# Optimization experiments

Measured on AMD Instinct MI355X. Metric: run time of the kernel, lower is better.

## Reference

```python
import jax, jax.numpy as jnp
import numpy as np

N = 50000
H = 256
EPS = 1e-5

def setup_inputs() -> dict:
    key = jax.random.key(0)
    ks = jax.random.split(key, 8)
    d = 128
    inp = {
        'x': jax.random.normal(ks[0], (N, d), jnp.float32),
        'edge_index': jax.random.randint(ks[1], (2, 800000), 0, N, jnp.int64),
        'W1': jax.random.normal(ks[2], (d, H), jnp.float32) * (2.0 / d) ** 0.5,
        'b1': jnp.zeros((H,), jnp.float32),
        'g1': jnp.ones((H,), jnp.float32),
        'be1': jnp.zeros((H,), jnp.float32),
        'W2': jax.random.normal(ks[3], (H, H), jnp.float32) * (2.0 / H) ** 0.5,
        'b2': jnp.zeros((H,), jnp.float32),
        'g2': jnp.ones((H,), jnp.float32),
        'be2': jnp.zeros((H,), jnp.float32),
        'W3': jax.random.normal(ks[4], (H, H), jnp.float32) * (2.0 / H) ** 0.5,
        'b3': jnp.zeros((H,), jnp.float32),
        'g3': jnp.ones((H,), jnp.float32),
        'be3': jnp.zeros((H,), jnp.float32),
        'Wf1': jax.random.normal(ks[5], (H, H // 2), jnp.float32) * (2.0 / H) ** 0.5,
        'bf1': jnp.zeros((H // 2,), jnp.float32),
        'Wf2': jax.random.normal(ks[6], (H // 2, 1), jnp.float32) * (2.0 / (H // 2)) ** 0.5,
        'bf2': jnp.zeros((1,), jnp.float32),
    }
    return inp

def _gcn_norm(edge_index):
    # add self-loops, symmetric normalization (PyG GCNConv defaults)
    loop = jnp.arange(N, dtype=edge_index.dtype)
    row = jnp.concatenate([edge_index[0], loop])  # source
    col = jnp.concatenate([edge_index[1], loop])  # target
    deg = jax.ops.segment_sum(jnp.ones_like(col, jnp.float32), col, num_segments=N)
    dis = jnp.where(deg > 0, jax.lax.rsqrt(deg), 0.0)
    norm = dis[row] * dis[col]  # [E+N]
    return row, col, norm

def _conv(x, W, b, row, col, norm):
    xw = x @ W                       # [N,H]
    msg = xw[row] * norm[:, None]    # gather + scale, [E+N,H]
    out = jax.ops.segment_sum(msg, col, num_segments=N)
    return out + b

def _ln(x, g, b):
    mu = jnp.mean(x, axis=-1, keepdims=True)
    var = jnp.var(x, axis=-1, keepdims=True)
    return (x - mu) * jax.lax.rsqrt(var + EPS) * g + b

def reference(x, edge_index, W1, b1, g1, be1, W2, b2, g2, be2, W3, b3, g3, be3, Wf1, bf1, Wf2, bf2):
    row, col, norm = _gcn_norm(edge_index)
    x1 = jax.nn.relu(_ln(_conv(x, W1, b1, row, col, norm), g1, be1))
    x2 = jax.nn.relu(_ln(_conv(x1, W2, b2, row, col, norm), g2, be2)) + 0.7 * x1
    x3 = jax.nn.relu(_ln(_conv(x2, W3, b3, row, col, norm), g3, be3)) * 0.7 + x2
    h = jax.nn.relu(x3 @ Wf1 + bf1)
    return h @ Wf2 + bf2  # [N,1]
```

## Files before the change

### kernel.cpp

```cpp
#include <hip/hip_runtime.h>
#include <cstdint>
#include <cstddef>

#define HDIM 256
#define DIN 128
#define EPSV 1e-5f
#define SCHUNK 1024

typedef __attribute__((ext_vector_type(8))) short short8;
typedef __attribute__((ext_vector_type(4))) float f32x4;

__device__ __forceinline__ float bf2f(unsigned int u16) {
  union { unsigned int i; float f; } v; v.i = u16 << 16; return v.f;
}
__device__ __forceinline__ unsigned short f2bf(float f) {
  union { float f; unsigned int i; } v; v.f = f;
  unsigned int u = v.i;
  return (unsigned short)((u + 0x7fffu + ((u >> 16) & 1u)) >> 16);
}
__device__ __forceinline__ float4 ldbf4(const unsigned short* p) {
  uint2 v = *(const uint2*)p;
  return make_float4(bf2f(v.x & 0xffffu), bf2f(v.x >> 16),
                     bf2f(v.y & 0xffffu), bf2f(v.y >> 16));
}
__device__ __forceinline__ void stbf4(unsigned short* p, float a, float b, float c, float d) {
  uint2 o;
  o.x = (unsigned int)f2bf(a) | ((unsigned int)f2bf(b) << 16);
  o.y = (unsigned int)f2bf(c) | ((unsigned int)f2bf(d) << 16);
  *(uint2*)p = o;
}

__global__ __launch_bounds__(256) void zero_i_k(int* deg, int* cur, int n) {
  int i = blockIdx.x * 256 + threadIdx.x;
  if (i < n) { deg[i] = 0; cur[i] = 0; }
}

__global__ __launch_bounds__(256) void hist_k(const int* __restrict__ col, int* deg, int e) {
  int i = blockIdx.x * 256 + threadIdx.x;
  if (i < e) atomicAdd(&deg[col[i]], 1);
}

__global__ __launch_bounds__(256) void scanA_k(const int* __restrict__ deg,
                                               int* __restrict__ row_ptr,
                                               int* __restrict__ blockSums,
                                               float* __restrict__ dis, int n) {
  __shared__ int waveSums[4];
  const int tid = threadIdx.x, lane = tid & 63, w = tid >> 6;
  const int base = blockIdx.x * SCHUNK + tid * 4;
  int v0 = 0, v1 = 0, v2 = 0, v3 = 0;
  if (base + 0 < n) v0 = deg[base + 0];
  if (base + 1 < n) v1 = deg[base + 1];
  if (base + 2 < n) v2 = deg[base + 2];
  if (base + 3 < n) v3 = deg[base + 3];
  if (base + 0 < n) dis[base + 0] = rsqrtf((float)(v0 + 1));
  if (base + 1 < n) dis[base + 1] = rsqrtf((float)(v1 + 1));
  if (base + 2 < n) dis[base + 2] = rsqrtf((float)(v2 + 1));
  if (base + 3 < n) dis[base + 3] = rsqrtf((float)(v3 + 1));
  int tsum = v0 + v1 + v2 + v3;
  int inc = tsum;
#pragma unroll
  for (int off = 1; off < 64; off <<= 1) {
    int t = __shfl_up(inc, off);
    if (lane >= off) inc += t;
  }
  if (lane == 63) waveSums[w] = inc;
  __syncthreads();
  int woff = 0;
#pragma unroll
  for (int k = 0; k < 4; ++k) woff += (k < w) ? waveSums[k] : 0;
  int excl = woff + inc - tsum;
  if (base + 0 < n) row_ptr[base + 0] = excl;
  if (base + 1 < n) row_ptr[base + 1] = excl + v0;
  if (base + 2 < n) row_ptr[base + 2] = excl + v0 + v1;
  if (base + 3 < n) row_ptr[base + 3] = excl + v0 + v1 + v2;
  if (tid == 255) blockSums[blockIdx.x] = woff + inc;
}

__global__ __launch_bounds__(256) void scanB_k(int* blockSums, int nb) {
  __shared__ int waveSums[4];
  const int tid = threadIdx.x, lane = tid & 63, w = tid >> 6;
  int v = (tid < nb) ? blockSums[tid] : 0;
  int inc = v;
#pragma unroll
  for (int off = 1; off < 64; off <<= 1) {
    int t = __shfl_up(inc, off);
    if (lane >= off) inc += t;
  }
  if (lane == 63) waveSums[w] = inc;
  __syncthreads();
  int woff = 0;
#pragma unroll
  for (int k = 0; k < 4; ++k) woff += (k < w) ? waveSums[k] : 0;
  if (tid < nb) blockSums[tid] = woff + inc - v;
}

__global__ __launch_bounds__(256) void scanC_k(int* __restrict__ row_ptr,
                                               const int* __restrict__ blockSums,
                                               int n, int e) {
  const int base = blockIdx.x * SCHUNK + threadIdx.x * 4;
  const int add = blockSums[blockIdx.x];
#pragma unroll
  for (int k = 0; k < 4; ++k)
    if (base + k < n) row_ptr[base + k] += add;
  if (blockIdx.x == 0 && threadIdx.x == 0) row_ptr[n] = e;
}

__global__ __launch_bounds__(256) void fill_k(const int* __restrict__ row,
                                              const int* __restrict__ col,
                                              const int* __restrict__ row_ptr,
                                              int* cur, int* srcs, int e) {
  int i = blockIdx.x * 256 + threadIdx.x;
  if (i < e) {
    int c = col[i];
    int p = row_ptr[c] + atomicAdd(&cur[c], 1);
    srcs[p] = row[i];
  }
}

__global__ __launch_bounds__(256) void pack_k(const float* __restrict__ W,
                                              unsigned short* __restrict__ out,
                                              int K, int C) {
  int idx = blockIdx.x * 256 + threadIdx.x;
  if (idx >= K * C) return;
  int j = idx & 7, lane = (idx >> 3) & 63, rest = idx >> 9;
  int NSUB = C >> 4;
  int ns = rest % NSUB, kb = rest / NSUB;
  int k = kb * 32 + (lane >> 4) * 8 + j;
  int c = ns * 16 + (lane & 15);
  out[idx] = f2bf(W[(size_t)k * C + c]);
}

__global__ __launch_bounds__(256) void cvt_k(const float* __restrict__ in,
                                             unsigned short* __restrict__ out, int tot) {
  int i = blockIdx.x * 256 + threadIdx.x;
  if (i < tot) out[i] = f2bf(in[i]);
}

template<int MODE, int K, int CN>
__global__ __launch_bounds__(256) void gemm_k(
    const unsigned short* __restrict__ A, const unsigned short* __restrict__ Wp,
    unsigned short* __restrict__ out, const float* __restrict__ sb, int n) {
  constexpr int NSUB = CN / 16;
  constexpr int KC = K / 32;
  const int t = threadIdx.x;
  const int w = t >> 6, lane = t & 63;
  const int rg = w & 1, cg = w >> 1;
  const int g = lane >> 4, i = lane & 15;
  const int m0 = blockIdx.x * 64 + rg * 32;
  const int nsBase = blockIdx.y * 8 + cg * 4;

  const int r0 = m0 + i, r1 = m0 + 16 + i;
  const int l0 = r0 < n ? r0 : n - 1;
  const int l1 = r1 < n ? r1 : n - 1;
  const unsigned short* a0 = A + (size_t)l0 * K + g * 8;
  const unsigned short* a1 = A + (size_t)l1 * K + g * 8;
  const short8* wp = (const short8*)Wp + (size_t)nsBase * 64 + lane;

  f32x4 acc[2][4];
#pragma unroll
  for (int rr = 0; rr < 2; ++rr)
#pragma unroll
    for (int j = 0; j < 4; ++j) acc[rr][j] = (f32x4){0.f, 0.f, 0.f, 0.f};

  short8 af0 = *(const short8*)a0;
  short8 af1 = *(const short8*)a1;
  short8 wf[4];
#pragma unroll
  for (int j = 0; j < 4; ++j) wf[j] = wp[j * 64];

#pragma unroll
  for (int kc = 0; kc < KC; ++kc) {
    short8 naf0, naf1, nwf[4];
    if (kc + 1 < KC) {
      naf0 = *(const short8*)(a0 + (kc + 1) * 32);
      naf1 = *(const short8*)(a1 + (kc + 1) * 32);
#pragma unroll
      for (int j = 0; j < 4; ++j) nwf[j] = wp[(size_t)(kc + 1) * NSUB * 64 + j * 64];
    }
#pragma unroll
    for (int j = 0; j < 4; ++j) {
      acc[0][j] = __builtin_amdgcn_mfma_f32_16x16x32_bf16(wf[j], af0, acc[0][j], 0, 0, 0);
      acc[1][j] = __builtin_amdgcn_mfma_f32_16x16x32_bf16(wf[j], af1, acc[1][j], 0, 0, 0);
    }
    if (kc + 1 < KC) {
      af0 = naf0; af1 = naf1;
#pragma unroll
      for (int j = 0; j < 4; ++j) wf[j] = nwf[j];
    }
  }

#pragma unroll
  for (int rr = 0; rr < 2; ++rr) {
    int r = m0 + rr * 16 + i;
    if (r < n) {
      unsigned short* op = out + (size_t)r * CN + nsBase * 16 + g * 4;
      if (MODE == 0) {
        float s = sb[r];
#pragma unroll
        for (int j = 0; j < 4; ++j)
          stbf4(op + j * 16, acc[rr][j][0] * s, acc[rr][j][1] * s,
                acc[rr][j][2] * s, acc[rr][j][3] * s);
      } else {
#pragma unroll
        for (int j = 0; j < 4; ++j) {
          float4 b4 = *(const float4*)(sb + nsBase * 16 + j * 16 + g * 4);
          stbf4(op + j * 16,
                fmaxf(acc[rr][j][0] + b4.x, 0.f), fmaxf(acc[rr][j][1] + b4.y, 0.f),
                fmaxf(acc[rr][j][2] + b4.z, 0.f), fmaxf(acc[rr][j][3] + b4.w, 0.f));
        }
      }
    }
  }
}

template<int MODE>
__global__ __launch_bounds__(256) void gather_ln_k(
    const unsigned short* __restrict__ xws, const int* __restrict__ row_ptr,
    const int* __restrict__ srcs, const float* __restrict__ dis,
    const float* __restrict__ bias, const float* __restrict__ g,
    const float* __restrict__ be, const unsigned short* __restrict__ xprev,
    unsigned short* __restrict__ out, int n) {
  int i = blockIdx.x * 4 + (threadIdx.x >> 6);
  int lane = threadIdx.x & 63;
  if (i >= n) return;
  int beg = row_ptr[i], end = row_ptr[i + 1];
  const int co = lane * 4;
  float4 acc = ldbf4(xws + (size_t)i * HDIM + co);
  int j = beg;
  for (; j + 8 <= end; j += 8) {
    int r0 = srcs[j], r1 = srcs[j + 1], r2 = srcs[j + 2], r3 = srcs[j + 3];
    int r4 = srcs[j + 4], r5 = srcs[j + 5], r6 = srcs[j + 6], r7 = srcs[j + 7];
    float4 v0 = ldbf4(xws + (size_t)r0 * HDIM + co);
    float4 v1 = ldbf4(xws + (size_t)r1 * HDIM + co);
    float4 v2 = ldbf4(xws + (size_t)r2 * HDIM + co);
    float4 v3 = ldbf4(xws + (size_t)r3 * HDIM + co);
    float4 v4 = ldbf4(xws + (size_t)r4 * HDIM + co);
    float4 v5 = ldbf4(xws + (size_t)r5 * HDIM + co);
    float4 v6 = ldbf4(xws + (size_t)r6 * HDIM + co);
    float4 v7 = ldbf4(xws + (size_t)r7 * HDIM + co);
    acc.x += ((v0.x + v1.x) + (v2.x + v3.x)) + ((v4.x + v5.x) + (v6.x + v7.x));
    acc.y += ((v0.y + v1.y) + (v2.y + v3.y)) + ((v4.y + v5.y) + (v6.y + v7.y));
    acc.z += ((v0.z + v1.z) + (v2.z + v3.z)) + ((v4.z + v5.z) + (v6.z + v7.z));
    acc.w += ((v0.w + v1.w) + (v2.w + v3.w)) + ((v4.w + v5.w) + (v6.w + v7.w));
  }
  for (; j + 4 <= end; j += 4) {
    int r0 = srcs[j], r1 = srcs[j + 1], r2 = srcs[j + 2], r3 = srcs[j + 3];
    float4 v0 = ldbf4(xws + (size_t)r0 * HDIM + co);
    float4 v1 = ldbf4(xws + (size_t)r1 * HDIM + co);
    float4 v2 = ldbf4(xws + (size_t)r2 * HDIM + co);
    float4 v3 = ldbf4(xws + (size_t)r3 * HDIM + co);
    acc.x += (v0.x + v1.x) + (v2.x + v3.x);
    acc.y += (v0.y + v1.y) + (v2.y + v3.y);
    acc.z += (v0.z + v1.z) + (v2.z + v3.z);
    acc.w += (v0.w + v1.w) + (v2.w + v3.w);
  }
  for (; j < end; ++j) {
    float4 v = ldbf4(xws + (size_t)srcs[j] * HDIM + co);
    acc.x += v.x; acc.y += v.y; acc.z += v.z; acc.w += v.w;
  }
  float di = dis[i];
  float4 b4 = *(const float4*)(bias + co);
  float4 v;
  v.x = acc.x * di + b4.x;
  v.y = acc.y * di + b4.y;
  v.z = acc.z * di + b4.z;
  v.w = acc.w * di + b4.w;
  float s = v.x + v.y + v.z + v.w;
  float s2 = v.x * v.x + v.y * v.y + v.z * v.z + v.w * v.w;
#pragma unroll
  for (int off = 1; off < 64; off <<= 1) {
    s += __shfl_xor(s, off);
    s2 += __shfl_xor(s2, off);
  }
  float mu = s * (1.f / HDIM);
  float inv = rsqrtf(s2 * (1.f / HDIM) - mu * mu + EPSV);
  float4 g4 = *(const float4*)(g + co);
  float4 e4 = *(const float4*)(be + co);
  float4 o;
  o.x = fmaxf((v.x - mu) * inv * g4.x + e4.x, 0.f);
  o.y = fmaxf((v.y - mu) * inv * g4.y + e4.y, 0.f);
  o.z = fmaxf((v.z - mu) * inv * g4.z + e4.z, 0.f);
  o.w = fmaxf((v.w - mu) * inv * g4.w + e4.w, 0.f);
  if (MODE == 1) {
    float4 p = ldbf4(xprev + (size_t)i * HDIM + co);
    o.x += 0.7f * p.x; o.y += 0.7f * p.y; o.z += 0.7f * p.z; o.w += 0.7f * p.w;
  } else if (MODE == 2) {
    float4 p = ldbf4(xprev + (size_t)i * HDIM + co);
    o.x = o.x * 0.7f + p.x; o.y = o.y * 0.7f + p.y;
    o.z = o.z * 0.7f + p.z; o.w = o.w * 0.7f + p.w;
  }
  stbf4(out + (size_t)i * HDIM + co, o.x, o.y, o.z, o.w);
}

__global__ __launch_bounds__(256) void dot_k(
    const unsigned short* __restrict__ h, const float* __restrict__ w,
    const float* __restrict__ bf2, float* __restrict__ out, int n) {
  int i = blockIdx.x * 4 + (threadIdx.x >> 6);
  int lane = threadIdx.x & 63;
  if (i >= n) return;
  unsigned int hv = *(const unsigned int*)(h + (size_t)i * 128 + lane * 2);
  float2 wv = *(const float2*)(w + lane * 2);
  float p = bf2f(hv & 0xffffu) * wv.x + bf2f(hv >> 16) * wv.y;
#pragma unroll
  for (int off = 1; off < 64; off <<= 1) p += __shfl_xor(p, off);
  if (lane == 0) out[i] = p + bf2[0];
}

extern "C" void kernel_launch(void* const* d_in, const int* in_sizes, int n_in,
                              void* d_out, int out_size, void* d_ws, size_t ws_size,
                              hipStream_t stream) {
  const float* x   = (const float*)d_in[0];
  const int*   ei  = (const int*)d_in[1];
  const float* W1  = (const float*)d_in[2];
  const float* b1  = (const float*)d_in[3];
  const float* g1  = (const float*)d_in[4];
  const float* be1 = (const float*)d_in[5];
  const float* W2  = (const float*)d_in[6];
  const float* b2  = (const float*)d_in[7];
  const float* g2  = (const float*)d_in[8];
  const float* be2 = (const float*)d_in[9];
  const float* W3  = (const float*)d_in[10];
  const float* b3  = (const float*)d_in[11];
  const float* g3  = (const float*)d_in[12];
  const float* be3 = (const float*)d_in[13];
  const float* Wf1 = (const float*)d_in[14];
  const float* bf1 = (const float*)d_in[15];
  const float* Wf2 = (const float*)d_in[16];
  const float* bf2 = (const float*)d_in[17];
  float* out = (float*)d_out;

  const int n = in_sizes[0] / DIN;
  const int e = in_sizes[1] / 2;
  const int* row = ei;
  const int* col = ei + e;

  char* ws = (char*)d_ws;
  size_t off = 0;
  auto alloc = [&](size_t bytes) -> void* {
    void* p = ws + off;
    off = (off + bytes + 255) & ~(size_t)255;
    return p;
  };
  float*          dis     = (float*)alloc((size_t)n * 4);
  int*            deg_i   = (int*)alloc((size_t)n * 4);
  int*            cur     = (int*)alloc((size_t)n * 4);
  int*            row_ptr = (int*)alloc((size_t)(n + 1) * 4);
  int*            bsums   = (int*)alloc((size_t)256 * 4);
  int*            srcs    = (int*)alloc((size_t)e * 4);
  unsigned short* W1p     = (unsigned short*)alloc((size_t)DIN * HDIM * 2);
  unsigned short* W2p     = (unsigned short*)alloc((size_t)HDIM * HDIM * 2);
  unsigned short* W3p     = (unsigned short*)alloc((size_t)HDIM * HDIM * 2);
  unsigned short* Wf1p    = (unsigned short*)alloc((size_t)HDIM * 128 * 2);
  unsigned short* xbf     = (unsigned short*)alloc((size_t)n * DIN * 2);
  unsigned short* xws     = (unsigned short*)alloc((size_t)n * HDIM * 2);
  unsigned short* x1      = (unsigned short*)alloc((size_t)n * HDIM * 2);
  unsigned short* x2      = (unsigned short*)alloc((size_t)n * HDIM * 2);
  unsigned short* x3      = x1;
  unsigned short* h       = xbf;

  const int nb  = (n + 255) / 256;
  const int eb  = (e + 255) / 256;
  const int lnb = (n + 3) / 4;
  const int sb_ = (n + SCHUNK - 1) / SCHUNK;
  dim3 gg((n + 63) / 64, 2);
  dim3 gh((n + 63) / 64, 1);

  zero_i_k<<<nb, 256, 0, stream>>>(deg_i, cur, n);
  hist_k<<<eb, 256, 0, stream>>>(col, deg_i, e);
  scanA_k<<<sb_, 256, 0, stream>>>(deg_i, row_ptr, bsums, dis, n);
  scanB_k<<<1, 256, 0, stream>>>(bsums, sb_);
  scanC_k<<<sb_, 256, 0, stream>>>(row_ptr, bsums, n, e);
  fill_k<<<eb, 256, 0, stream>>>(row, col, row_ptr, cur, srcs, e);

  pack_k<<<(DIN * HDIM + 255) / 256, 256, 0, stream>>>(W1, W1p, DIN, HDIM);
  pack_k<<<(HDIM * HDIM + 255) / 256, 256, 0, stream>>>(W2, W2p, HDIM, HDIM);
  pack_k<<<(HDIM * HDIM + 255) / 256, 256, 0, stream>>>(W3, W3p, HDIM, HDIM);
  pack_k<<<(HDIM * 128 + 255) / 256, 256, 0, stream>>>(Wf1, Wf1p, HDIM, 128);
  cvt_k<<<(n * DIN + 255) / 256, 256, 0, stream>>>(x, xbf, n * DIN);

  gemm_k<0, DIN, HDIM><<<gg, 256, 0, stream>>>(xbf, W1p, xws, dis, n);
  gather_ln_k<0><<<lnb, 256, 0, stream>>>(xws, row_ptr, srcs, dis, b1, g1, be1, nullptr, x1, n);

  gemm_k<0, HDIM, HDIM><<<gg, 256, 0, stream>>>(x1, W2p, xws, dis, n);
  gather_ln_k<1><<<lnb, 256, 0, stream>>>(xws, row_ptr, srcs, dis, b2, g2, be2, x1, x2, n);

  gemm_k<0, HDIM, HDIM><<<gg, 256, 0, stream>>>(x2, W3p, xws, dis, n);
  gather_ln_k<2><<<lnb, 256, 0, stream>>>(xws, row_ptr, srcs, dis, b3, g3, be3, x2, x3, n);

  gemm_k<1, HDIM, 128><<<gh, 256, 0, stream>>>(x3, Wf1p, h, bf1, n);
  dot_k<<<lnb, 256, 0, stream>>>(h, Wf2, bf2, out, n);
}
```

Baseline: 486.2 us.

## Aggregate before GEMM and fuse LayerNorm and final MLP into GEMM epilogues

```diff
diff --git a/kernel.cpp b/kernel.cpp
--- a/kernel.cpp
+++ b/kernel.cpp
@@ -117,11 +117,9 @@
   }
 }
 
-__global__ __launch_bounds__(256) void pack_k(const float* __restrict__ W,
-                                              unsigned short* __restrict__ out,
-                                              int K, int C) {
-  int idx = blockIdx.x * 256 + threadIdx.x;
-  if (idx >= K * C) return;
+__device__ __forceinline__ void packW(const float* __restrict__ W,
+                                      unsigned short* __restrict__ out,
+                                      int idx, int C) {
   int j = idx & 7, lane = (idx >> 3) & 63, rest = idx >> 9;
   int NSUB = C >> 4;
   int ns = rest % NSUB, kb = rest / NSUB;
@@ -130,180 +128,285 @@
   out[idx] = f2bf(W[(size_t)k * C + c]);
 }
 
-__global__ __launch_bounds__(256) void cvt_k(const float* __restrict__ in,
-                                             unsigned short* __restrict__ out, int tot) {
-  int i = blockIdx.x * 256 + threadIdx.x;
-  if (i < tot) out[i] = f2bf(in[i]);
-}
-
-template<int MODE, int K, int CN>
-__global__ __launch_bounds__(256) void gemm_k(
-    const unsigned short* __restrict__ A, const unsigned short* __restrict__ Wp,
-    unsigned short* __restrict__ out, const float* __restrict__ sb, int n) {
-  constexpr int NSUB = CN / 16;
-  constexpr int KC = K / 32;
-  const int t = threadIdx.x;
-  const int w = t >> 6, lane = t & 63;
-  const int rg = w & 1, cg = w >> 1;
-  const int g = lane >> 4, i = lane & 15;
-  const int m0 = blockIdx.x * 64 + rg * 32;
-  const int nsBase = blockIdx.y * 8 + cg * 4;
-
-  const int r0 = m0 + i, r1 = m0 + 16 + i;
-  const int l0 = r0 < n ? r0 : n - 1;
-  const int l1 = r1 < n ? r1 : n - 1;
-  const unsigned short* a0 = A + (size_t)l0 * K + g * 8;
-  const unsigned short* a1 = A + (size_t)l1 * K + g * 8;
-  const short8* wp = (const short8*)Wp + (size_t)nsBase * 64 + lane;
-
-  f32x4 acc[2][4];
-#pragma unroll
-  for (int rr = 0; rr < 2; ++rr)
-#pragma unroll
-    for (int j = 0; j < 4; ++j) acc[rr][j] = (f32x4){0.f, 0.f, 0.f, 0.f};
-
-  short8 af0 = *(const short8*)a0;
-  short8 af1 = *(const short8*)a1;
-  short8 wf[4];
-#pragma unroll
-  for (int j = 0; j < 4; ++j) wf[j] = wp[j * 64];
-
-#pragma unroll
-  for (int kc = 0; kc < KC; ++kc) {
-    short8 naf0, naf1, nwf[4];
-    if (kc + 1 < KC) {
-      naf0 = *(const short8*)(a0 + (kc + 1) * 32);
-      naf1 = *(const short8*)(a1 + (kc + 1) * 32);
-#pragma unroll
-      for (int j = 0; j < 4; ++j) nwf[j] = wp[(size_t)(kc + 1) * NSUB * 64 + j * 64];
-    }
-#pragma unroll
-    for (int j = 0; j < 4; ++j) {
-      acc[0][j] = __builtin_amdgcn_mfma_f32_16x16x32_bf16(wf[j], af0, acc[0][j], 0, 0, 0);
-      acc[1][j] = __builtin_amdgcn_mfma_f32_16x16x32_bf16(wf[j], af1, acc[1][j], 0, 0, 0);
-    }
-    if (kc + 1 < KC) {
-      af0 = naf0; af1 = naf1;
-#pragma unroll
-      for (int j = 0; j < 4; ++j) wf[j] = nwf[j];
-    }
-  }
-
-#pragma unroll
-  for (int rr = 0; rr < 2; ++rr) {
-    int r = m0 + rr * 16 + i;
-    if (r < n) {
-      unsigned short* op = out + (size_t)r * CN + nsBase * 16 + g * 4;
-      if (MODE == 0) {
-        float s = sb[r];
-#pragma unroll
-        for (int j = 0; j < 4; ++j)
-          stbf4(op + j * 16, acc[rr][j][0] * s, acc[rr][j][1] * s,
-                acc[rr][j][2] * s, acc[rr][j][3] * s);
-      } else {
-#pragma unroll
-        for (int j = 0; j < 4; ++j) {
-          float4 b4 = *(const float4*)(sb + nsBase * 16 + j * 16 + g * 4);
-          stbf4(op + j * 16,
-                fmaxf(acc[rr][j][0] + b4.x, 0.f), fmaxf(acc[rr][j][1] + b4.y, 0.f),
-                fmaxf(acc[rr][j][2] + b4.z, 0.f), fmaxf(acc[rr][j][3] + b4.w, 0.f));
-        }
-      }
-    }
-  }
-}
-
-template<int MODE>
-__global__ __launch_bounds__(256) void gather_ln_k(
-    const unsigned short* __restrict__ xws, const int* __restrict__ row_ptr,
+__global__ __launch_bounds__(256) void prep_k(
+    const float* __restrict__ W1, const float* __restrict__ W2,
+    const float* __restrict__ W3, const float* __restrict__ Wf1,
+    const float* __restrict__ x,
+    unsigned short* __restrict__ W1p, unsigned short* __restrict__ W2p,
+    unsigned short* __restrict__ W3p, unsigned short* __restrict__ Wf1p,
+    unsigned short* __restrict__ xbf, int nx) {
+  int idx = blockIdx.x * 256 + threadIdx.x;
+  const int s0 = DIN * HDIM, s1 = s0 + HDIM * HDIM, s2 = s1 + HDIM * HDIM,
+            s3 = s2 + HDIM * 128;
+  if (idx < s0) packW(W1, W1p, idx, HDIM);
+  else if (idx < s1) packW(W2, W2p, idx - s0, HDIM);
+  else if (idx < s2) packW(W3, W3p, idx - s1, HDIM);
+  else if (idx < s3) packW(Wf1, Wf1p, idx - s2, 128);
+  else if (idx - s3 < nx) xbf[idx - s3] = f2bf(x[idx - s3]);
+}
+
+__global__ __launch_bounds__(256) void gather256_k(
+    const unsigned short* __restrict__ x, const int* __restrict__ row_ptr,
     const int* __restrict__ srcs, const float* __restrict__ dis,
-    const float* __restrict__ bias, const float* __restrict__ g,
-    const float* __restrict__ be, const unsigned short* __restrict__ xprev,
     unsigned short* __restrict__ out, int n) {
   int i = blockIdx.x * 4 + (threadIdx.x >> 6);
   int lane = threadIdx.x & 63;
   if (i >= n) return;
   int beg = row_ptr[i], end = row_ptr[i + 1];
   const int co = lane * 4;
-  float4 acc = ldbf4(xws + (size_t)i * HDIM + co);
+  float di = dis[i];
+  float4 sv = ldbf4(x + (size_t)i * 256 + co);
+  float4 acc = make_float4(di * sv.x, di * sv.y, di * sv.z, di * sv.w);
   int j = beg;
   for (; j + 8 <= end; j += 8) {
     int r0 = srcs[j], r1 = srcs[j + 1], r2 = srcs[j + 2], r3 = srcs[j + 3];
     int r4 = srcs[j + 4], r5 = srcs[j + 5], r6 = srcs[j + 6], r7 = srcs[j + 7];
-    float4 v0 = ldbf4(xws + (size_t)r0 * HDIM + co);
-    float4 v1 = ldbf4(xws + (size_t)r1 * HDIM + co);
-    float4 v2 = ldbf4(xws + (size_t)r2 * HDIM + co);
-    float4 v3 = ldbf4(xws + (size_t)r3 * HDIM + co);
-    float4 v4 = ldbf4(xws + (size_t)r4 * HDIM + co);
-    float4 v5 = ldbf4(xws + (size_t)r5 * HDIM + co);
-    float4 v6 = ldbf4(xws + (size_t)r6 * HDIM + co);
-    float4 v7 = ldbf4(xws + (size_t)r7 * HDIM + co);
-    acc.x += ((v0.x + v1.x) + (v2.x + v3.x)) + ((v4.x + v5.x) + (v6.x + v7.x));
-    acc.y += ((v0.y + v1.y) + (v2.y + v3.y)) + ((v4.y + v5.y) + (v6.y + v7.y));
-    acc.z += ((v0.z + v1.z) + (v2.z + v3.z)) + ((v4.z + v5.z) + (v6.z + v7.z));
-    acc.w += ((v0.w + v1.w) + (v2.w + v3.w)) + ((v4.w + v5.w) + (v6.w + v7.w));
-  }
-  for (; j + 4 <= end; j += 4) {
-    int r0 = srcs[j], r1 = srcs[j + 1], r2 = srcs[j + 2], r3 = srcs[j + 3];
-    float4 v0 = ldbf4(xws + (size_t)r0 * HDIM + co);
-    float4 v1 = ldbf4(xws + (size_t)r1 * HDIM + co);
-    float4 v2 = ldbf4(xws + (size_t)r2 * HDIM + co);
-    float4 v3 = ldbf4(xws + (size_t)r3 * HDIM + co);
-    acc.x += (v0.x + v1.x) + (v2.x + v3.x);
-    acc.y += (v0.y + v1.y) + (v2.y + v3.y);
-    acc.z += (v0.z + v1.z) + (v2.z + v3.z);
-    acc.w += (v0.w + v1.w) + (v2.w + v3.w);
+    float d0 = dis[r0], d1 = dis[r1], d2 = dis[r2], d3 = dis[r3];
+    float d4 = dis[r4], d5 = dis[r5], d6 = dis[r6], d7 = dis[r7];
+    float4 v0 = ldbf4(x + (size_t)r0 * 256 + co);
+    float4 v1 = ldbf4(x + (size_t)r1 * 256 + co);
+    float4 v2 = ldbf4(x + (size_t)r2 * 256 + co);
+    float4 v3 = ldbf4(x + (size_t)r3 * 256 + co);
+    float4 v4 = ldbf4(x + (size_t)r4 * 256 + co);
+    float4 v5 = ldbf4(x + (size_t)r5 * 256 + co);
+    float4 v6 = ldbf4(x + (size_t)r6 * 256 + co);
+    float4 v7 = ldbf4(x + (size_t)r7 * 256 + co);
+    acc.x += ((d0*v0.x + d1*v1.x) + (d2*v2.x + d3*v3.x)) + ((d4*v4.x + d5*v5.x) + (d6*v6.x + d7*v7.x));
+    acc.y += ((d0*v0.y + d1*v1.y) + (d2*v2.y + d3*v3.y)) + ((d4*v4.y + d5*v5.y) + (d6*v6.y + d7*v7.y));
+    acc.z += ((d0*v0.z + d1*v1.z) + (d2*v2.z + d3*v3.z)) + ((d4*v4.z + d5*v5.z) + (d6*v6.z + d7*v7.z));
+    acc.w += ((d0*v0.w + d1*v1.w) + (d2*v2.w + d3*v3.w)) + ((d4*v4.w + d5*v5.w) + (d6*v6.w + d7*v7.w));
   }
   for (; j < end; ++j) {
-    float4 v = ldbf4(xws + (size_t)srcs[j] * HDIM + co);
-    acc.x += v.x; acc.y += v.y; acc.z += v.z; acc.w += v.w;
-  }
-  float di = dis[i];
-  float4 b4 = *(const float4*)(bias + co);
-  float4 v;
-  v.x = acc.x * di + b4.x;
-  v.y = acc.y * di + b4.y;
-  v.z = acc.z * di + b4.z;
-  v.w = acc.w * di + b4.w;
-  float s = v.x + v.y + v.z + v.w;
-  float s2 = v.x * v.x + v.y * v.y + v.z * v.z + v.w * v.w;
-#pragma unroll
-  for (int off = 1; off < 64; off <<= 1) {
-    s += __shfl_xor(s, off);
-    s2 += __shfl_xor(s2, off);
-  }
-  float mu = s * (1.f / HDIM);
-  float inv = rsqrtf(s2 * (1.f / HDIM) - mu * mu + EPSV);
-  float4 g4 = *(const float4*)(g + co);
-  float4 e4 = *(const float4*)(be + co);
-  float4 o;
-  o.x = fmaxf((v.x - mu) * inv * g4.x + e4.x, 0.f);
-  o.y = fmaxf((v.y - mu) * inv * g4.y + e4.y, 0.f);
-  o.z = fmaxf((v.z - mu) * inv * g4.z + e4.z, 0.f);
-  o.w = fmaxf((v.w - mu) * inv * g4.w + e4.w, 0.f);
-  if (MODE == 1) {
-    float4 p = ldbf4(xprev + (size_t)i * HDIM + co);
-    o.x += 0.7f * p.x; o.y += 0.7f * p.y; o.z += 0.7f * p.z; o.w += 0.7f * p.w;
-  } else if (MODE == 2) {
-    float4 p = ldbf4(xprev + (size_t)i * HDIM + co);
-    o.x = o.x * 0.7f + p.x; o.y = o.y * 0.7f + p.y;
-    o.z = o.z * 0.7f + p.z; o.w = o.w * 0.7f + p.w;
-  }
-  stbf4(out + (size_t)i * HDIM + co, o.x, o.y, o.z, o.w);
-}
-
-__global__ __launch_bounds__(256) void dot_k(
-    const unsigned short* __restrict__ h, const float* __restrict__ w,
-    const float* __restrict__ bf2, float* __restrict__ out, int n) {
+    int r = srcs[j];
+    float d = dis[r];
+    float4 v = ldbf4(x + (size_t)r * 256 + co);
+    acc.x += d * v.x; acc.y += d * v.y; acc.z += d * v.z; acc.w += d * v.w;
+  }
+  stbf4(out + (size_t)i * 256 + co, di * acc.x, di * acc.y, di * acc.z, di * acc.w);
+}
+
+__global__ __launch_bounds__(256) void gather128_k(
+    const unsigned short* __restrict__ x, const int* __restrict__ row_ptr,
+    const int* __restrict__ srcs, const float* __restrict__ dis,
+    unsigned short* __restrict__ out, int n) {
   int i = blockIdx.x * 4 + (threadIdx.x >> 6);
   int lane = threadIdx.x & 63;
   if (i >= n) return;
-  unsigned int hv = *(const unsigned int*)(h + (size_t)i * 128 + lane * 2);
-  float2 wv = *(const float2*)(w + lane * 2);
-  float p = bf2f(hv & 0xffffu) * wv.x + bf2f(hv >> 16) * wv.y;
-#pragma unroll
-  for (int off = 1; off < 64; off <<= 1) p += __shfl_xor(p, off);
-  if (lane == 0) out[i] = p + bf2[0];
+  int beg = row_ptr[i], end = row_ptr[i + 1];
+  const int co = lane * 2;
+  float di = dis[i];
+  unsigned int sv = *(const unsigned int*)(x + (size_t)i * 128 + co);
+  float ax = di * bf2f(sv & 0xffffu), ay = di * bf2f(sv >> 16);
+  int j = beg;
+  for (; j + 8 <= end; j += 8) {
+    int r0 = srcs[j], r1 = srcs[j + 1], r2 = srcs[j + 2], r3 = srcs[j + 3];
+    int r4 = srcs[j + 4], r5 = srcs[j + 5], r6 = srcs[j + 6], r7 = srcs[j + 7];
+    float d0 = dis[r0], d1 = dis[r1], d2 = dis[r2], d3 = dis[r3];
+    float d4 = dis[r4], d5 = dis[r5], d6 = dis[r6], d7 = dis[r7];
+    unsigned int u0 = *(const unsigned int*)(x + (size_t)r0 * 128 + co);
+    unsigned int u1 = *(const unsigned int*)(x + (size_t)r1 * 128 + co);
+    unsigned int u2 = *(const unsigned int*)(x + (size_t)r2 * 128 + co);
+    unsigned int u3 = *(const unsigned int*)(x + (size_t)r3 * 128 + co);
+    unsigned int u4 = *(const unsigned int*)(x + (size_t)r4 * 128 + co);
+    unsigned int u5 = *(const unsigned int*)(x + (size_t)r5 * 128 + co);
+    unsigned int u6 = *(const unsigned int*)(x + (size_t)r6 * 128 + co);
+    unsigned int u7 = *(const unsigned int*)(x + (size_t)r7 * 128 + co);
+    ax += ((d0*bf2f(u0&0xffffu) + d1*bf2f(u1&0xffffu)) + (d2*bf2f(u2&0xffffu) + d3*bf2f(u3&0xffffu)))
+        + ((d4*bf2f(u4&0xffffu) + d5*bf2f(u5&0xffffu)) + (d6*bf2f(u6&0xffffu) + d7*bf2f(u7&0xffffu)));
+    ay += ((d0*bf2f(u0>>16) + d1*bf2f(u1>>16)) + (d2*bf2f(u2>>16) + d3*bf2f(u3>>16)))
+        + ((d4*bf2f(u4>>16) + d5*bf2f(u5>>16)) + (d6*bf2f(u6>>16) + d7*bf2f(u7>>16)));
+  }
+  for (; j < end; ++j) {
+    int r = srcs[j];
+    float d = dis[r];
+    unsigned int u = *(const unsigned int*)(x + (size_t)r * 128 + co);
+    ax += d * bf2f(u & 0xffffu);
+    ay += d * bf2f(u >> 16);
+  }
+  unsigned int o = (unsigned int)f2bf(di * ax) | ((unsigned int)f2bf(di * ay) << 16);
+  *(unsigned int*)(out + (size_t)i * 128 + co) = o;
+}
+
+template<int MODE, int K>
+__global__ __launch_bounds__(512) void gemmln_k(
+    const unsigned short* __restrict__ A, const unsigned short* __restrict__ Wp,
+    const float* __restrict__ bias, const float* __restrict__ gam,
+    const float* __restrict__ bet, const unsigned short* __restrict__ xprev,
+    unsigned short* __restrict__ out, int n) {
+  constexpr int CN = 256, NSUB = 16, KC = K / 32;
+  __shared__ float red_s[64][4], red_q[64][4];
+  const int t = threadIdx.x;
+  const int w = t >> 6, lane = t & 63;
+  const int rg = w & 1, cg = w >> 1;
+  const int gq = lane >> 4, i = lane & 15;
+  const int m0 = blockIdx.x * 64;
+  const int r0 = m0 + rg * 32 + i, r1 = r0 + 16;
+  const int l0 = r0 < n ? r0 : n - 1, l1 = r1 < n ? r1 : n - 1;
+  const unsigned short* a0 = A + (size_t)l0 * K + gq * 8;
+  const unsigned short* a1 = A + (size_t)l1 * K + gq * 8;
+  const short8* wp = (const short8*)Wp + (size_t)(cg * 4) * 64 + lane;
+
+  f32x4 acc[2][4];
+#pragma unroll
+  for (int rr = 0; rr < 2; ++rr)
+#pragma unroll
+    for (int j = 0; j < 4; ++j) acc[rr][j] = (f32x4){0.f, 0.f, 0.f, 0.f};
+
+  short8 af0 = *(const short8*)a0;
+  short8 af1 = *(const short8*)a1;
+  short8 wf[4];
+#pragma unroll
+  for (int j = 0; j < 4; ++j) wf[j] = wp[j * 64];
+
+#pragma unroll
+  for (int kc = 0; kc < KC; ++kc) {
+    short8 naf0, naf1, nwf[4];
+    if (kc + 1 < KC) {
+      naf0 = *(const short8*)(a0 + (kc + 1) * 32);
+      naf1 = *(const short8*)(a1 + (kc + 1) * 32);
+#pragma unroll
+      for (int j = 0; j < 4; ++j) nwf[j] = wp[(size_t)(kc + 1) * NSUB * 64 + j * 64];
+    }
+#pragma unroll
+    for (int j = 0; j < 4; ++j) {
+      acc[0][j] = __builtin_amdgcn_mfma_f32_16x16x32_bf16(wf[j], af0, acc[0][j], 0, 0, 0);
+      acc[1][j] = __builtin_amdgcn_mfma_f32_16x16x32_bf16(wf[j], af1, acc[1][j], 0, 0, 0);
+    }
+    if (kc + 1 < KC) {
+      af0 = naf0; af1 = naf1;
+#pragma unroll
+      for (int j = 0; j < 4; ++j) wf[j] = nwf[j];
+    }
+  }
+
+  const int colb = cg * 64 + gq * 4;
+  float s0 = 0.f, q0 = 0.f, s1 = 0.f, q1 = 0.f;
+#pragma unroll
+  for (int j = 0; j < 4; ++j) {
+    f32x4 b4 = *(const f32x4*)(bias + colb + j * 16);
+#pragma unroll
+    for (int r = 0; r < 4; ++r) {
+      acc[0][j][r] += b4[r];
+      acc[1][j][r] += b4[r];
+      float v = acc[0][j][r]; s0 += v; q0 += v * v;
+      float u = acc[1][j][r]; s1 += u; q1 += u * u;
+    }
+  }
+  s0 += __shfl_xor(s0, 16); s0 += __shfl_xor(s0, 32);
+  q0 += __shfl_xor(q0, 16); q0 += __shfl_xor(q0, 32);
+  s1 += __shfl_xor(s1, 16); s1 += __shfl_xor(s1, 32);
+  q1 += __shfl_xor(q1, 16); q1 += __shfl_xor(q1, 32);
+  if (gq == 0) {
+    red_s[rg * 32 + i][cg] = s0;      red_q[rg * 32 + i][cg] = q0;
+    red_s[rg * 32 + 16 + i][cg] = s1; red_q[rg * 32 + 16 + i][cg] = q1;
+  }
+  __syncthreads();
+
+#pragma unroll
+  for (int rr = 0; rr < 2; ++rr) {
+    int il = rg * 32 + rr * 16 + i;
+    int r = m0 + il;
+    if (r >= n) continue;
+    float ss = (red_s[il][0] + red_s[il][1]) + (red_s[il][2] + red_s[il][3]);
+    float qq = (red_q[il][0] + red_q[il][1]) + (red_q[il][2] + red_q[il][3]);
+    float mu = ss * (1.f / CN);
+    float inv = rsqrtf(qq * (1.f / CN) - mu * mu + EPSV);
+    unsigned short* op = out + (size_t)r * CN + colb;
+    const unsigned short* pp = (MODE != 0) ? (xprev + (size_t)r * CN + colb) : nullptr;
+#pragma unroll
+    for (int j = 0; j < 4; ++j) {
+      f32x4 g4 = *(const f32x4*)(gam + colb + j * 16);
+      f32x4 e4 = *(const f32x4*)(bet + colb + j * 16);
+      float o0 = fmaxf((acc[rr][j][0] - mu) * inv * g4[0] + e4[0], 0.f);
+      float o1 = fmaxf((acc[rr][j][1] - mu) * inv * g4[1] + e4[1], 0.f);
+      float o2 = fmaxf((acc[rr][j][2] - mu) * inv * g4[2] + e4[2], 0.f);
+      float o3 = fmaxf((acc[rr][j][3] - mu) * inv * g4[3] + e4[3], 0.f);
+      if (MODE == 1) {
+        float4 pv = ldbf4(pp + j * 16);
+        o0 += 0.7f * pv.x; o1 += 0.7f * pv.y; o2 += 0.7f * pv.z; o3 += 0.7f * pv.w;
+      } else if (MODE == 2) {
+        float4 pv = ldbf4(pp + j * 16);
+        o0 = o0 * 0.7f + pv.x; o1 = o1 * 0.7f + pv.y;
+        o2 = o2 * 0.7f + pv.z; o3 = o3 * 0.7f + pv.w;
+      }
+      stbf4(op + j * 16, o0, o1, o2, o3);
+    }
+  }
+}
+
+__global__ __launch_bounds__(256) void gemmdot_k(
+    const unsigned short* __restrict__ A, const unsigned short* __restrict__ Wp,
+    const float* __restrict__ b1, const float* __restrict__ w2,
+    const float* __restrict__ b2, float* __restrict__ out, int n) {
+  constexpr int K = 256, NSUB = 8, KC = 8;
+  __shared__ float redh[64][2];
+  const int t = threadIdx.x;
+  const int w = t >> 6, lane = t & 63;
+  const int rg = w & 1, cg = w >> 1;
+  const int gq = lane >> 4, i = lane & 15;
+  const int m0 = blockIdx.x * 64;
+  const int r0 = m0 + rg * 32 + i, r1 = r0 + 16;
+  const int l0 = r0 < n ? r0 : n - 1, l1 = r1 < n ? r1 : n - 1;
+  const unsigned short* a0 = A + (size_t)l0 * K + gq * 8;
+  const unsigned short* a1 = A + (size_t)l1 * K + gq * 8;
+  const short8* wp = (const short8*)Wp + (size_t)(cg * 4) * 64 + lane;
+
+  f32x4 acc[2][4];
+#pragma unroll
+  for (int rr = 0; rr < 2; ++rr)
+#pragma unroll
+    for (int j = 0; j < 4; ++j) acc[rr][j] = (f32x4){0.f, 0.f, 0.f, 0.f};
+
+  short8 af0 = *(const short8*)a0;
+  short8 af1 = *(const short8*)a1;
+  short8 wf[4];
+#pragma unroll
+  for (int j = 0; j < 4; ++j) wf[j] = wp[j * 64];
+
+#pragma unroll
+  for (int kc = 0; kc < KC; ++kc) {
+    short8 naf0, naf1, nwf[4];
+    if (kc + 1 < KC) {
+      naf0 = *(const short8*)(a0 + (kc + 1) * 32);
+      naf1 = *(const short8*)(a1 + (kc + 1) * 32);
+#pragma unroll
+      for (int j = 0; j < 4; ++j) nwf[j] = wp[(size_t)(kc + 1) * NSUB * 64 + j * 64];
+    }
+#pragma unroll
+    for (int j = 0; j < 4; ++j) {
+      acc[0][j] = __builtin_amdgcn_mfma_f32_16x16x32_bf16(wf[j], af0, acc[0][j], 0, 0, 0);
+      acc[1][j] = __builtin_amdgcn_mfma_f32_16x16x32_bf16(wf[j], af1, acc[1][j], 0, 0, 0);
+    }
+    if (kc + 1 < KC) {
+      af0 = naf0; af1 = naf1;
+#pragma unroll
+      for (int j = 0; j < 4; ++j) wf[j] = nwf[j];
+    }
+  }
+
+  const int colb = cg * 64 + gq * 4;
+  float p0 = 0.f, p1 = 0.f;
+#pragma unroll
+  for (int j = 0; j < 4; ++j) {
+    f32x4 bb = *(const f32x4*)(b1 + colb + j * 16);
+    f32x4 ww = *(const f32x4*)(w2 + colb + j * 16);
+#pragma unroll
+    for (int r = 0; r < 4; ++r) {
+      p0 += fmaxf(acc[0][j][r] + bb[r], 0.f) * ww[r];
+      p1 += fmaxf(acc[1][j][r] + bb[r], 0.f) * ww[r];
+    }
+  }
+  p0 += __shfl_xor(p0, 16); p0 += __shfl_xor(p0, 32);
+  p1 += __shfl_xor(p1, 16); p1 += __shfl_xor(p1, 32);
+  if (gq == 0) {
+    redh[rg * 32 + i][cg] = p0;
+    redh[rg * 32 + 16 + i][cg] = p1;
+  }
+  __syncthreads();
+  if (t < 64) {
+    int r = m0 + t;
+    if (r < n) out[r] = redh[t][0] + redh[t][1] + b2[0];
+  }
 }
 
 extern "C" void kernel_launch(void* const* d_in, const int* in_sizes, int n_in,
@@ -352,18 +455,18 @@
   unsigned short* W3p     = (unsigned short*)alloc((size_t)HDIM * HDIM * 2);
   unsigned short* Wf1p    = (unsigned short*)alloc((size_t)HDIM * 128 * 2);
   unsigned short* xbf     = (unsigned short*)alloc((size_t)n * DIN * 2);
-  unsigned short* xws     = (unsigned short*)alloc((size_t)n * HDIM * 2);
+  unsigned short* agg     = (unsigned short*)alloc((size_t)n * HDIM * 2);
   unsigned short* x1      = (unsigned short*)alloc((size_t)n * HDIM * 2);
   unsigned short* x2      = (unsigned short*)alloc((size_t)n * HDIM * 2);
+  unsigned short* a1      = agg;
   unsigned short* x3      = x1;
-  unsigned short* h       = xbf;
 
   const int nb  = (n + 255) / 256;
   const int eb  = (e + 255) / 256;
   const int lnb = (n + 3) / 4;
+  const int gb  = (n + 63) / 64;
   const int sb_ = (n + SCHUNK - 1) / SCHUNK;
-  dim3 gg((n + 63) / 64, 2);
-  dim3 gh((n + 63) / 64, 1);
+  const int prep_tot = DIN * HDIM + HDIM * HDIM + HDIM * HDIM + HDIM * 128 + n * DIN;
 
   zero_i_k<<<nb, 256, 0, stream>>>(deg_i, cur, n);
   hist_k<<<eb, 256, 0, stream>>>(col, deg_i, e);
@@ -372,21 +475,17 @@
   scanC_k<<<sb_, 256, 0, stream>>>(row_ptr, bsums, n, e);
   fill_k<<<eb, 256, 0, stream>>>(row, col, row_ptr, cur, srcs, e);
 
-  pack_k<<<(DIN * HDIM + 255) / 256, 256, 0, stream>>>(W1, W1p, DIN, HDIM);
-  pack_k<<<(HDIM * HDIM + 255) / 256, 256, 0, stream>>>(W2, W2p, HDIM, HDIM);
-  pack_k<<<(HDIM * HDIM + 255) / 256, 256, 0, stream>>>(W3, W3p, HDIM, HDIM);
-  pack_k<<<(HDIM * 128 + 255) / 256, 256, 0, stream>>>(Wf1, Wf1p, HDIM, 128);
-  cvt_k<<<(n * DIN + 255) / 256, 256, 0, stream>>>(x, xbf, n * DIN);
-
-  gemm_k<0, DIN, HDIM><<<gg, 256, 0, stream>>>(xbf, W1p, xws, dis, n);
-  gather_ln_k<0><<<lnb, 256, 0, stream>>>(xws, row_ptr, srcs, dis, b1, g1, be1, nullptr, x1, n);
-
-  gemm_k<0, HDIM, HDIM><<<gg, 256, 0, stream>>>(x1, W2p, xws, dis, n);
-  gather_ln_k<1><<<lnb, 256, 0, stream>>>(xws, row_ptr, srcs, dis, b2, g2, be2, x1, x2, n);
-
-  gemm_k<0, HDIM, HDIM><<<gg, 256, 0, stream>>>(x2, W3p, xws, dis, n);
-  gather_ln_k<2><<<lnb, 256, 0, stream>>>(xws, row_ptr, srcs, dis, b3, g3, be3, x2, x3, n);
-
-  gemm_k<1, HDIM, 128><<<gh, 256, 0, stream>>>(x3, Wf1p, h, bf1, n);
-  dot_k<<<lnb, 256, 0, stream>>>(h, Wf2, bf2, out, n);
-}
+  prep_k<<<(prep_tot + 255) / 256, 256, 0, stream>>>(W1, W2, W3, Wf1, x,
+                                                     W1p, W2p, W3p, Wf1p, xbf, n * DIN);
+
+  gather128_k<<<lnb, 256, 0, stream>>>(xbf, row_ptr, srcs, dis, a1, n);
+  gemmln_k<0, DIN><<<gb, 512, 0, stream>>>(a1, W1p, b1, g1, be1, nullptr, x1, n);
+
+  gather256_k<<<lnb, 256, 0, stream>>>(x1, row_ptr, srcs, dis, agg, n);
+  gemmln_k<1, HDIM><<<gb, 512, 0, stream>>>(agg, W2p, b2, g2, be2, x1, x2, n);
+
+  gather256_k<<<lnb, 256, 0, stream>>>(x2, row_ptr, srcs, dis, agg, n);
+  gemmln_k<2, HDIM><<<gb, 512, 0, stream>>>(agg, W3p, b3, g3, be3, x2, x3, n);
+
+  gemmdot_k<<<gb, 256, 0, stream>>>(x3, Wf1p, bf1, Wf2, bf2, out, n);
+}
```

Result: faster. 470.6 us (-3.2%).
